# Optimization experiments

Measured on AMD Instinct MI355X. Metric: run time of the kernel, lower is better.

Reference implementation:

```python
import jax, jax.numpy as jnp
import numpy as np

N_NODES = 100000
N_EDGES = 1600000
IN_CH = 256
HID = 128   # latent_dim * 2
LAT = 64    # latent_dim


def _gcn_conv(x, W, b, src, dst, n_nodes):
    """PyG GCNConv: linear -> symmetric degree-norm scatter-add -> bias.
    src/dst already include self-loops."""
    h = x @ W.T                                             # [N, out]
    deg = jax.ops.segment_sum(jnp.ones_like(dst, dtype=h.dtype), dst,
                              num_segments=n_nodes)          # in-degree incl. self-loop
    dinv = jnp.where(deg > 0, jax.lax.rsqrt(deg), 0.0)
    norm = dinv[src] * dinv[dst]                             # [E]
    msg = h[src] * norm[:, None]                             # gather + scale, [E, out]
    out = jax.ops.segment_sum(msg, dst, num_segments=n_nodes)  # scatter-add
    return out + b


def setup_inputs() -> dict:
    key = jax.random.key(0)
    k1, k2, k3, k4, k5, k6 = jax.random.split(key, 6)
    x = jax.random.normal(k1, (N_NODES, IN_CH), dtype=jnp.float32)
    edge_index = jax.random.randint(k2, (2, N_EDGES), 0, N_NODES, dtype=jnp.int64)
    # Glorot-ish init for linear weights, zero bias (PyG default)
    W1 = jax.random.normal(k3, (HID, IN_CH), dtype=jnp.float32) / np.sqrt(IN_CH)
    b1 = jnp.zeros((HID,), dtype=jnp.float32)
    W2 = jax.random.normal(k4, (LAT, HID), dtype=jnp.float32) / np.sqrt(HID)
    b2 = jnp.zeros((LAT,), dtype=jnp.float32)
    return {"x": x, "edge_index": edge_index, "W1": W1, "b1": b1, "W2": W2, "b2": b2}


def reference(x, edge_index, W1, b1, W2, b2):
    n = x.shape[0]
    # add self-loops (PyG GCNConv default add_self_loops=True)
    loop = jnp.arange(n, dtype=edge_index.dtype)
    src = jnp.concatenate([edge_index[0], loop])
    dst = jnp.concatenate([edge_index[1], loop])
    h = jax.nn.relu(_gcn_conv(x, W1, b1, src, dst, n))
    return _gcn_conv(h, W2, b2, src, dst, n)
```

## Files before the change

### kernel.cpp

```cpp
#include <hip/hip_runtime.h>
#include <math.h>

constexpr int IN_CH = 256;
constexpr int HID   = 128;
constexpr int LAT   = 64;

constexpr int SBN    = 1024;
constexpr int SB_CAP = 18432;
constexpr int EPB    = 8192;
constexpr int HCAP   = 9472;

typedef unsigned short u16;
typedef unsigned int   u32;
typedef unsigned char  u8;
typedef __bf16  bf16x8 __attribute__((ext_vector_type(8)));
typedef float   f32x4  __attribute__((ext_vector_type(4)));

__device__ inline u16 f2bf(float f) {
    unsigned u = __float_as_uint(f);
    unsigned r = u + 0x7FFF + ((u >> 16) & 1);
    return (u16)(r >> 16);
}
__device__ inline float bf2f(u16 h) {
    return __uint_as_float((unsigned)h << 16);
}


__global__ void k_zero(int* p, int n) {
    int i = blockIdx.x * blockDim.x + threadIdx.x;
    if (i < n) p[i] = 0;
}

__launch_bounds__(512)
__global__ void k_bin_sb(const int* __restrict__ esrc, const int* __restrict__ edst,
                         int* __restrict__ sb_fill, u32* __restrict__ sbe,
                         int E, int NSB) {
    __shared__ u32 sorted[EPB];
    __shared__ u8  ssb[EPB];
    __shared__ int cnt[128], sc[128], excl[128], fil[128], off[128];

    const int t  = threadIdx.x;
    const int e0 = blockIdx.x * EPB;

    for (int j = t; j < 128; j += 512) { cnt[j] = 0; fil[j] = 0; }
    __syncthreads();

#pragma unroll
    for (int it = 0; it < EPB / 512; ++it) {
        int e = e0 + it * 512 + t;
        if (e < E) atomicAdd(&cnt[edst[e] >> 10], 1);
    }
    __syncthreads();

    if (t < 128) sc[t] = cnt[t];
    __syncthreads();
#pragma unroll
    for (int o = 1; o < 128; o <<= 1) {
        int u = 0;
        if (t < 128 && t >= o) u = sc[t - o];
        __syncthreads();
        if (t < 128) sc[t] += u;
        __syncthreads();
    }
    if (t < 128) excl[t] = sc[t] - cnt[t];
    if (t < NSB) off[t] = atomicAdd(&sb_fill[t], cnt[t]);
    __syncthreads();

#pragma unroll
    for (int it = 0; it < EPB / 512; ++it) {
        int e = e0 + it * 512 + t;
        if (e < E) {
            int d  = edst[e];
            int sb = d >> 10;
            int pos = excl[sb] + atomicAdd(&fil[sb], 1);
            sorted[pos] = (u32)esrc[e] | ((u32)(d & 1023) << 17);
            ssb[pos]    = (u8)sb;
        }
    }
    __syncthreads();

    int mtot = sc[127];
    for (int i = t; i < mtot; i += 512) {
        int sb = ssb[i];
        int o  = off[sb] + (i - excl[sb]);
        if (o < SB_CAP) sbe[(size_t)sb * SB_CAP + o] = sorted[i];
    }
}

__launch_bounds__(512)
__global__ void k_sbsort(const int* __restrict__ sb_fill, const u32* __restrict__ sbe,
                         int* __restrict__ csr, int* __restrict__ row_ptr,
                         int* __restrict__ row_end, float* __restrict__ dinv, int N) {
    __shared__ int cnt[SBN];
    __shared__ int exclh[512];
    __shared__ int fillb[512];
    __shared__ int lsrc[HCAP];
    __shared__ int wsum[8];
    __shared__ int sh_h1base, sh_mtot;

    const int t    = threadIdx.x;
    const int sb   = blockIdx.x >> 1;
    const int half = blockIdx.x & 1;
    const int m    = min(sb_fill[sb], SB_CAP);
    const size_t base = (size_t)sb * SB_CAP;
    const int node0 = sb * SBN;

    for (int j = t; j < SBN; j += 512) cnt[j] = 0;
    fillb[t & 511] = 0;
    __syncthreads();

    for (int i = t; i < m; i += 512)
        atomicAdd(&cnt[sbe[base + i] >> 17], 1);
    __syncthreads();

    int c0 = cnt[2 * t], c1 = cnt[2 * t + 1];
    int p  = c0 + c1;
    int lane = t & 63, wid = t >> 6;
    int v = p;
#pragma unroll
    for (int o = 1; o < 64; o <<= 1) {
        int u = __shfl_up(v, o, 64);
        if (lane >= o) v += u;
    }
    if (lane == 63) wsum[wid] = v;
    __syncthreads();
    int woff = 0;
#pragma unroll
    for (int w = 0; w < 8; ++w) if (w < wid) woff += wsum[w];
    int incl = woff + v;
    int eP   = incl - p;
    if (t == 511) sh_mtot = incl;
    if (t == 256) sh_h1base = eP;

#pragma unroll
    for (int q = 0; q < 2; ++q) {
        int j  = 2 * t + q;
        int ex = q ? (eP + c0) : eP;
        int cc = q ? c1 : c0;
        if ((j >> 9) == half) {
            exclh[j & 511] = ex;
            int node = node0 + j;
            if (node < N) {
                row_ptr[node] = (int)base + ex;
                row_end[node] = (int)base + ex + cc;
                dinv[node]    = rsqrtf((float)(cc + 1));
            }
        }
    }
    __syncthreads();

    const int hb = (half == 0) ? 0 : sh_h1base;
    int mh = (half == 0) ? sh_h1base : (sh_mtot - sh_h1base);

    for (int i = t; i < m; i += 512) {
        u32 p2  = sbe[base + i];
        int d10 = p2 >> 17;
        if ((d10 >> 9) == half) {
            int slot = atomicAdd(&fillb[d10 & 511], 1);
            int pos  = exclh[d10 & 511] - hb + slot;
            if (pos < HCAP) lsrc[pos] = (int)(p2 & 0x1FFFF);
        }
    }
    __syncthreads();

    if (mh > HCAP) mh = HCAP;
    for (int i = t; i < mh; i += 512) csr[base + hb + i] = lsrc[i];
}


__global__ void k_split_w(const float* __restrict__ W, u16* __restrict__ Wh,
                          u16* __restrict__ Wl, int n) {
    int i = blockIdx.x * blockDim.x + threadIdx.x;
    if (i < n) {
        float v = W[i];
        u16 h = f2bf(v);
        Wh[i] = h;
        Wl[i] = f2bf(v - bf2f(h));
    }
}


template<int K, int NOUT, bool A_BF16, typename AT>
__device__ inline void gemm_body(int bid,
                                 const AT* __restrict__ A,
                                 const u16* __restrict__ Wh,
                                 const u16* __restrict__ Wl,
                                 const float* __restrict__ dinv,
                                 u16* __restrict__ h_out,
                                 int M) {
    constexpr int BM = 64, BK = 32, LDT = 40, THREADS = 512;
    constexpr int WAVES_N  = (NOUT == 128) ? 4 : 2;
    constexpr int WAVES_M  = 8 / WAVES_N;
    constexpr int WM       = BM / WAVES_M;
    constexpr int WN       = 32;
    constexpr int MF       = WM / 16;
    constexpr int NF       = WN / 16;

    __shared__ u16 Ah[BM][LDT];
    __shared__ u16 Al[A_BF16 ? 1 : BM][A_BF16 ? 1 : LDT];
    __shared__ u16 Bh[NOUT][LDT], Bl[NOUT][LDT];

    const int t    = threadIdx.x;
    const int lane = t & 63;
    const int wid  = t >> 6;
    const int wm   = (wid / WAVES_N) * WM;
    const int wn   = (wid % WAVES_N) * WN;
    const int lr   = lane & 15;
    const int lk   = (lane >> 4) * 8;
    const int row0 = bid * BM;

    f32x4 acc[MF][NF];
#pragma unroll
    for (int i = 0; i < MF; ++i)
#pragma unroll
        for (int j = 0; j < NF; ++j) acc[i][j] = (f32x4)(0.f);

    for (int k0 = 0; k0 < K; k0 += BK) {
        {
            int r  = t >> 3;
            int c4 = (t & 7) * 4;
            int gr = row0 + r;
            if (A_BF16) {
                ushort4 hv = make_ushort4(0, 0, 0, 0);
                if (gr < M) hv = *(const ushort4*)&((const u16*)A)[(size_t)gr * K + k0 + c4];
                *(ushort4*)&Ah[r][c4] = hv;
            } else {
                float4 v = make_float4(0.f, 0.f, 0.f, 0.f);
                if (gr < M) v = *(const float4*)&((const float*)A)[(size_t)gr * K + k0 + c4];
                ushort4 hi, lo;
                hi.x = f2bf(v.x); lo.x = f2bf(v.x - bf2f(hi.x));
                hi.y = f2bf(v.y); lo.y = f2bf(v.y - bf2f(hi.y));
                hi.z = f2bf(v.z); lo.z = f2bf(v.z - bf2f(hi.z));
                hi.w = f2bf(v.w); lo.w = f2bf(v.w - bf2f(hi.w));
                *(ushort4*)&Ah[r][c4] = hi;
                *(ushort4*)&Al[r][c4] = lo;
            }
        }
#pragma unroll
        for (int it = 0; it < (NOUT * BK / 4) / THREADS; ++it) {
            int q  = it * THREADS + t;
            int r  = q >> 3;
            int c4 = (q & 7) * 4;
            *(ushort4*)&Bh[r][c4] = *(const ushort4*)&Wh[(size_t)r * K + k0 + c4];
            *(ushort4*)&Bl[r][c4] = *(const ushort4*)&Wl[(size_t)r * K + k0 + c4];
        }
        __syncthreads();

        bf16x8 ah[MF], al[MF], bh[NF], bl[NF];
#pragma unroll
        for (int mf = 0; mf < MF; ++mf) {
            ah[mf] = *(const bf16x8*)&Ah[wm + mf * 16 + lr][lk];
            if (!A_BF16) al[mf] = *(const bf16x8*)&Al[wm + mf * 16 + lr][lk];
        }
#pragma unroll
        for (int nf = 0; nf < NF; ++nf) {
            bh[nf] = *(const bf16x8*)&Bh[wn + nf * 16 + lr][lk];
            bl[nf] = *(const bf16x8*)&Bl[wn + nf * 16 + lr][lk];
        }
#pragma unroll
        for (int mf = 0; mf < MF; ++mf)
#pragma unroll
            for (int nf = 0; nf < NF; ++nf) {
                acc[mf][nf] = __builtin_amdgcn_mfma_f32_16x16x32_bf16(ah[mf], bh[nf], acc[mf][nf], 0, 0, 0);
                acc[mf][nf] = __builtin_amdgcn_mfma_f32_16x16x32_bf16(ah[mf], bl[nf], acc[mf][nf], 0, 0, 0);
                if (!A_BF16)
                    acc[mf][nf] = __builtin_amdgcn_mfma_f32_16x16x32_bf16(al[mf], bh[nf], acc[mf][nf], 0, 0, 0);
            }
        __syncthreads();
    }

#pragma unroll
    for (int mf = 0; mf < MF; ++mf) {
#pragma unroll
        for (int r = 0; r < 4; ++r) {
            int grow = row0 + wm + mf * 16 + (lane >> 4) * 4 + r;
            if (grow < M) {
                float dv = dinv[grow];
#pragma unroll
                for (int nf = 0; nf < NF; ++nf)
                    h_out[(size_t)grow * NOUT + wn + nf * 16 + lr] = f2bf(acc[mf][nf][r] * dv);
            }
        }
    }
}

__launch_bounds__(512, 4)
__global__ void k_gemm1(const float* __restrict__ A,
                        const u16* __restrict__ Wh, const u16* __restrict__ Wl,
                        const float* __restrict__ dinv, u16* __restrict__ h_out, int M) {
    gemm_body<IN_CH, HID, false>(blockIdx.x, A, Wh, Wl, dinv, h_out, M);
}

__launch_bounds__(512, 4)
__global__ void k_gemm2(const u16* __restrict__ A,
                        const u16* __restrict__ Wh, const u16* __restrict__ Wl,
                        const float* __restrict__ dinv, u16* __restrict__ h_out, int M) {
    gemm_body<HID, LAT, true>(blockIdx.x, A, Wh, Wl, dinv, h_out, M);
}


__device__ inline void acc8(float* a, uint4 v) {
    a[0] += __uint_as_float(v.x << 16);
    a[1] += __uint_as_float(v.x & 0xFFFF0000u);
    a[2] += __uint_as_float(v.y << 16);
    a[3] += __uint_as_float(v.y & 0xFFFF0000u);
    a[4] += __uint_as_float(v.z << 16);
    a[5] += __uint_as_float(v.z & 0xFFFF0000u);
    a[6] += __uint_as_float(v.w << 16);
    a[7] += __uint_as_float(v.w & 0xFFFF0000u);
}

template<int C, bool RELU, bool OUT_BF16>
__global__ void k_aggregate(const int* __restrict__ row_ptr,
                            const int* __restrict__ row_end,
                            const int* __restrict__ csr,
                            const u16* __restrict__ h,
                            const float* __restrict__ dinv,
                            const float* __restrict__ bias,
                            void* __restrict__ out_v, int n) {
    constexpr int QSHIFT = (C == 128) ? 4 : 3;
    long long tid = (long long)blockIdx.x * blockDim.x + threadIdx.x;
    int node = (int)(tid >> QSHIFT);
    if (node >= n) return;
    int c = ((int)tid & ((1 << QSHIFT) - 1)) * 8;

    int k   = row_ptr[node];
    int end = row_end[node];

    float a[8] = {0.f, 0.f, 0.f, 0.f, 0.f, 0.f, 0.f, 0.f};
    acc8(a, *(const uint4*)&h[(size_t)node * C + c]);

    for (; k + 8 <= end; k += 8) {
        int s0 = csr[k],     s1 = csr[k + 1], s2 = csr[k + 2], s3 = csr[k + 3];
        int s4 = csr[k + 4], s5 = csr[k + 5], s6 = csr[k + 6], s7 = csr[k + 7];
        uint4 v0 = *(const uint4*)&h[(size_t)s0 * C + c];
        uint4 v1 = *(const uint4*)&h[(size_t)s1 * C + c];
        uint4 v2 = *(const uint4*)&h[(size_t)s2 * C + c];
        uint4 v3 = *(const uint4*)&h[(size_t)s3 * C + c];
        uint4 v4 = *(const uint4*)&h[(size_t)s4 * C + c];
        uint4 v5 = *(const uint4*)&h[(size_t)s5 * C + c];
        uint4 v6 = *(const uint4*)&h[(size_t)s6 * C + c];
        uint4 v7 = *(const uint4*)&h[(size_t)s7 * C + c];
        acc8(a, v0); acc8(a, v1); acc8(a, v2); acc8(a, v3);
        acc8(a, v4); acc8(a, v5); acc8(a, v6); acc8(a, v7);
    }
    if (k + 4 <= end) {
        int s0 = csr[k], s1 = csr[k + 1], s2 = csr[k + 2], s3 = csr[k + 3];
        uint4 v0 = *(const uint4*)&h[(size_t)s0 * C + c];
        uint4 v1 = *(const uint4*)&h[(size_t)s1 * C + c];
        uint4 v2 = *(const uint4*)&h[(size_t)s2 * C + c];
        uint4 v3 = *(const uint4*)&h[(size_t)s3 * C + c];
        acc8(a, v0); acc8(a, v1); acc8(a, v2); acc8(a, v3);
        k += 4;
    }
    for (; k < end; ++k) {
        int s0 = csr[k];
        acc8(a, *(const uint4*)&h[(size_t)s0 * C + c]);
    }

    float dvn = dinv[node];
    float4 b0 = *(const float4*)&bias[c];
    float4 b1 = *(const float4*)&bias[c + 4];
    float o[8];
    o[0] = fmaf(a[0], dvn, b0.x);
    o[1] = fmaf(a[1], dvn, b0.y);
    o[2] = fmaf(a[2], dvn, b0.z);
    o[3] = fmaf(a[3], dvn, b0.w);
    o[4] = fmaf(a[4], dvn, b1.x);
    o[5] = fmaf(a[5], dvn, b1.y);
    o[6] = fmaf(a[6], dvn, b1.z);
    o[7] = fmaf(a[7], dvn, b1.w);
    if (RELU) {
#pragma unroll
        for (int j = 0; j < 8; ++j) o[j] = fmaxf(o[j], 0.f);
    }
    if (OUT_BF16) {
        u16 r[8];
#pragma unroll
        for (int j = 0; j < 8; ++j) r[j] = f2bf(o[j]);
        *(uint4*)&((u16*)out_v)[(size_t)node * C + c] = *(const uint4*)r;
    } else {
        float* out = (float*)out_v;
        *(f32x4*)&out[(size_t)node * C + c]     = *(const f32x4*)&o[0];
        *(f32x4*)&out[(size_t)node * C + c + 4] = *(const f32x4*)&o[4];
    }
}


extern "C" void kernel_launch(void* const* d_in, const int* in_sizes, int n_in,
                              void* d_out, int out_size, void* d_ws, size_t ws_size,
                              hipStream_t stream) {
    const float* x   = (const float*)d_in[0];
    const int*   ei  = (const int*)d_in[1];
    const float* W1  = (const float*)d_in[2];
    const float* b1  = (const float*)d_in[3];
    const float* W2  = (const float*)d_in[4];
    const float* b2  = (const float*)d_in[5];
    float*       out = (float*)d_out;

    const int N = in_sizes[0] / IN_CH;
    const int E = in_sizes[1] / 2;
    const int* esrc = ei;
    const int* edst = ei + E;

    const int NSB = (N + SBN - 1) / SBN;
    const int NBB = (E + EPB - 1) / EPB;
    const int GB  = (N + 63) / 64;

    char* ws = (char*)d_ws;
    int*   sb_fill = (int*)ws;    ws += (size_t)((NSB + 31) & ~31) * 4;
    u32*   sbe     = (u32*)ws;    ws += (size_t)NSB * SB_CAP * 4;
    int*   csr     = (int*)ws;    ws += (size_t)NSB * SB_CAP * 4;
    int*   row_ptr = (int*)ws;    ws += (size_t)N * 4;
    int*   row_end = (int*)ws;    ws += (size_t)N * 4;
    float* dinv    = (float*)ws;  ws += (size_t)N * 4;
    u16*   W1h     = (u16*)ws;    ws += (size_t)HID * IN_CH * 2;
    u16*   W1l     = (u16*)ws;    ws += (size_t)HID * IN_CH * 2;
    u16*   W2h     = (u16*)ws;    ws += (size_t)LAT * HID * 2;
    u16*   W2l     = (u16*)ws;    ws += (size_t)LAT * HID * 2;
    u16*   h1      = (u16*)ws;    ws += (size_t)N * HID * 2;
    u16*   h2      = (u16*)ws;    ws += (size_t)N * LAT * 2;
    u16*   out1    = (u16*)ws;    ws += (size_t)N * HID * 2;

    dim3 blk(256);

    k_zero   <<<1, 128, 0, stream>>>(sb_fill, NSB);
    k_split_w<<<(HID * IN_CH + 255) / 256, blk, 0, stream>>>(W1, W1h, W1l, HID * IN_CH);
    k_split_w<<<(LAT * HID + 255) / 256, blk, 0, stream>>>(W2, W2h, W2l, LAT * HID);

    k_bin_sb<<<NBB, dim3(512), 0, stream>>>(esrc, edst, sb_fill, sbe, E, NSB);
    k_sbsort<<<NSB * 2, dim3(512), 0, stream>>>(sb_fill, sbe, csr, row_ptr, row_end, dinv, N);

    k_gemm1<<<GB, dim3(512), 0, stream>>>(x, W1h, W1l, dinv, h1, N);
    {
        long long tot = (long long)N * 16;
        k_aggregate<HID, true, true><<<(unsigned)((tot + 255) / 256), blk, 0, stream>>>(
            row_ptr, row_end, csr, h1, dinv, b1, out1, N);
    }

    k_gemm2<<<GB, dim3(512), 0, stream>>>(out1, W2h, W2l, dinv, h2, N);
    {
        long long tot = (long long)N * 8;
        k_aggregate<LAT, false, false><<<(unsigned)((tot + 255) / 256), blk, 0, stream>>>(
            row_ptr, row_end, csr, h2, dinv, b2, out, N);
    }
}
```

Measured before the change: 197.6 us.

## Double-buffer GEMM shared-memory tiles with register prefetch of next K tile

The GEMM K loop now keeps two shared-memory buffers and loads the next K tile from global memory into registers before the current tile's MFMA work, writing it to the other buffer afterward. This hides global load latency behind matrix math and removes one barrier per iteration. In exchange it doubles LDS use and raises register pressure, which could lower occupancy under the 512-thread, 4-block launch bounds. The GEMM is likely only part of total time, since the scatter/gather stages probably dominate.

```diff
diff --git a/kernel.cpp b/kernel.cpp
--- a/kernel.cpp
+++ b/kernel.cpp
@@ -195,10 +195,11 @@
     constexpr int WN       = 32;
     constexpr int MF       = WM / 16;
     constexpr int NF       = WN / 16;
-
-    __shared__ u16 Ah[BM][LDT];
-    __shared__ u16 Al[A_BF16 ? 1 : BM][A_BF16 ? 1 : LDT];
-    __shared__ u16 Bh[NOUT][LDT], Bl[NOUT][LDT];
+    constexpr int BIT      = (NOUT * BK / 4) / THREADS;
+
+    __shared__ u16 AhS[2][BM][LDT];
+    __shared__ u16 AlS[A_BF16 ? 1 : 2][A_BF16 ? 1 : BM][A_BF16 ? 1 : LDT];
+    __shared__ u16 BhS[2][NOUT][LDT], BlS[2][NOUT][LDT];
 
     const int t    = threadIdx.x;
     const int lane = t & 63;
@@ -209,53 +210,79 @@
     const int lk   = (lane >> 4) * 8;
     const int row0 = bid * BM;
 
+    const int ar  = t >> 3;
+    const int ac4 = (t & 7) * 4;
+    const int gr  = row0 + ar;
+
     f32x4 acc[MF][NF];
 #pragma unroll
     for (int i = 0; i < MF; ++i)
 #pragma unroll
         for (int j = 0; j < NF; ++j) acc[i][j] = (f32x4)(0.f);
 
-    for (int k0 = 0; k0 < K; k0 += BK) {
-        {
-            int r  = t >> 3;
-            int c4 = (t & 7) * 4;
-            int gr = row0 + r;
-            if (A_BF16) {
-                ushort4 hv = make_ushort4(0, 0, 0, 0);
-                if (gr < M) hv = *(const ushort4*)&((const u16*)A)[(size_t)gr * K + k0 + c4];
-                *(ushort4*)&Ah[r][c4] = hv;
-            } else {
-                float4 v = make_float4(0.f, 0.f, 0.f, 0.f);
-                if (gr < M) v = *(const float4*)&((const float*)A)[(size_t)gr * K + k0 + c4];
-                ushort4 hi, lo;
-                hi.x = f2bf(v.x); lo.x = f2bf(v.x - bf2f(hi.x));
-                hi.y = f2bf(v.y); lo.y = f2bf(v.y - bf2f(hi.y));
-                hi.z = f2bf(v.z); lo.z = f2bf(v.z - bf2f(hi.z));
-                hi.w = f2bf(v.w); lo.w = f2bf(v.w - bf2f(hi.w));
-                *(ushort4*)&Ah[r][c4] = hi;
-                *(ushort4*)&Al[r][c4] = lo;
-            }
-        }
-#pragma unroll
-        for (int it = 0; it < (NOUT * BK / 4) / THREADS; ++it) {
+    float4  av;
+    ushort4 ahv;
+    ushort4 bhv[BIT], blv[BIT];
+
+    auto load_tile = [&](int k0) {
+        if constexpr (A_BF16) {
+            ahv = make_ushort4(0, 0, 0, 0);
+            if (gr < M) ahv = *(const ushort4*)&((const u16*)A)[(size_t)gr * K + k0 + ac4];
+        } else {
+            av = make_float4(0.f, 0.f, 0.f, 0.f);
+            if (gr < M) av = *(const float4*)&((const float*)A)[(size_t)gr * K + k0 + ac4];
+        }
+#pragma unroll
+        for (int it = 0; it < BIT; ++it) {
             int q  = it * THREADS + t;
             int r  = q >> 3;
             int c4 = (q & 7) * 4;
-            *(ushort4*)&Bh[r][c4] = *(const ushort4*)&Wh[(size_t)r * K + k0 + c4];
-            *(ushort4*)&Bl[r][c4] = *(const ushort4*)&Wl[(size_t)r * K + k0 + c4];
-        }
-        __syncthreads();
+            bhv[it] = *(const ushort4*)&Wh[(size_t)r * K + k0 + c4];
+            blv[it] = *(const ushort4*)&Wl[(size_t)r * K + k0 + c4];
+        }
+    };
+    auto write_tile = [&](int buf) {
+        if constexpr (A_BF16) {
+            *(ushort4*)&AhS[buf][ar][ac4] = ahv;
+        } else {
+            ushort4 hi, lo;
+            hi.x = f2bf(av.x); lo.x = f2bf(av.x - bf2f(hi.x));
+            hi.y = f2bf(av.y); lo.y = f2bf(av.y - bf2f(hi.y));
+            hi.z = f2bf(av.z); lo.z = f2bf(av.z - bf2f(hi.z));
+            hi.w = f2bf(av.w); lo.w = f2bf(av.w - bf2f(hi.w));
+            *(ushort4*)&AhS[buf][ar][ac4] = hi;
+            *(ushort4*)&AlS[buf][ar][ac4] = lo;
+        }
+#pragma unroll
+        for (int it = 0; it < BIT; ++it) {
+            int q  = it * THREADS + t;
+            int r  = q >> 3;
+            int c4 = (q & 7) * 4;
+            *(ushort4*)&BhS[buf][r][c4] = bhv[it];
+            *(ushort4*)&BlS[buf][r][c4] = blv[it];
+        }
+    };
+
+    load_tile(0);
+    write_tile(0);
+    __syncthreads();
+
+    int cur = 0;
+    for (int k0 = 0; k0 < K; k0 += BK) {
+        const bool have_next = (k0 + BK < K);
+        if (have_next) load_tile(k0 + BK);
 
         bf16x8 ah[MF], al[MF], bh[NF], bl[NF];
 #pragma unroll
         for (int mf = 0; mf < MF; ++mf) {
-            ah[mf] = *(const bf16x8*)&Ah[wm + mf * 16 + lr][lk];
-            if (!A_BF16) al[mf] = *(const bf16x8*)&Al[wm + mf * 16 + lr][lk];
+            ah[mf] = *(const bf16x8*)&AhS[cur][wm + mf * 16 + lr][lk];
+            if constexpr (!A_BF16)
+                al[mf] = *(const bf16x8*)&AlS[cur][wm + mf * 16 + lr][lk];
         }
 #pragma unroll
         for (int nf = 0; nf < NF; ++nf) {
-            bh[nf] = *(const bf16x8*)&Bh[wn + nf * 16 + lr][lk];
-            bl[nf] = *(const bf16x8*)&Bl[wn + nf * 16 + lr][lk];
+            bh[nf] = *(const bf16x8*)&BhS[cur][wn + nf * 16 + lr][lk];
+            bl[nf] = *(const bf16x8*)&BlS[cur][wn + nf * 16 + lr][lk];
         }
 #pragma unroll
         for (int mf = 0; mf < MF; ++mf)
@@ -263,10 +290,13 @@
             for (int nf = 0; nf < NF; ++nf) {
                 acc[mf][nf] = __builtin_amdgcn_mfma_f32_16x16x32_bf16(ah[mf], bh[nf], acc[mf][nf], 0, 0, 0);
                 acc[mf][nf] = __builtin_amdgcn_mfma_f32_16x16x32_bf16(ah[mf], bl[nf], acc[mf][nf], 0, 0, 0);
-                if (!A_BF16)
+                if constexpr (!A_BF16)
                     acc[mf][nf] = __builtin_amdgcn_mfma_f32_16x16x32_bf16(al[mf], bh[nf], acc[mf][nf], 0, 0, 0);
             }
+
+        if (have_next) write_tile(cur ^ 1);
         __syncthreads();
+        cur ^= 1;
     }
 
 #pragma unroll
```

Measured after the change: 199.4 us. No clear change (+0.9%).

## Keep GCN weights resident in LDS with persistent per-wave 16-row GEMM strips

Applied to the files above, without the earlier changes.

The two tiled GEMM kernels are replaced by one persistent kernel. Each 1024-thread block loads the whole split (high/low bf16) weight matrix into LDS once. Each wave then loops over 16-row strips, reading A straight from global memory into registers with a one-step software prefetch. This removes the repeated per-tile staging of weights and A through LDS and the per-k barriers. In exchange, gemm1 needs a large LDS footprint (about 135 KB), which limits occupancy to one block per CU, and A reads become per-lane row fragments rather than coalesced tile loads.

```diff
diff --git a/kernel.cpp b/kernel.cpp
--- a/kernel.cpp
+++ b/kernel.cpp
@@ -181,121 +181,103 @@
 
 
 template<int K, int NOUT, bool A_BF16, typename AT>
-__device__ inline void gemm_body(int bid,
-                                 const AT* __restrict__ A,
-                                 const u16* __restrict__ Wh,
-                                 const u16* __restrict__ Wl,
-                                 const float* __restrict__ dinv,
-                                 u16* __restrict__ h_out,
-                                 int M) {
-    constexpr int BM = 64, BK = 32, LDT = 40, THREADS = 512;
-    constexpr int WAVES_N  = (NOUT == 128) ? 4 : 2;
-    constexpr int WAVES_M  = 8 / WAVES_N;
-    constexpr int WM       = BM / WAVES_M;
-    constexpr int WN       = 32;
-    constexpr int MF       = WM / 16;
-    constexpr int NF       = WN / 16;
-
-    __shared__ u16 Ah[BM][LDT];
-    __shared__ u16 Al[A_BF16 ? 1 : BM][A_BF16 ? 1 : LDT];
-    __shared__ u16 Bh[NOUT][LDT], Bl[NOUT][LDT];
+__launch_bounds__(1024, 4)
+__global__ void k_gemm_wres(const AT* __restrict__ A,
+                            const u16* __restrict__ Wh,
+                            const u16* __restrict__ Wl,
+                            const float* __restrict__ dinv,
+                            u16* __restrict__ h_out,
+                            int M) {
+    constexpr int LDK = K + 8;
+    constexpr int NF  = NOUT / 16;
+
+    __shared__ u16 Bh[NOUT][LDK], Bl[NOUT][LDK];
 
     const int t    = threadIdx.x;
     const int lane = t & 63;
     const int wid  = t >> 6;
-    const int wm   = (wid / WAVES_N) * WM;
-    const int wn   = (wid % WAVES_N) * WN;
     const int lr   = lane & 15;
     const int lk   = (lane >> 4) * 8;
-    const int row0 = bid * BM;
-
-    f32x4 acc[MF][NF];
-#pragma unroll
-    for (int i = 0; i < MF; ++i)
-#pragma unroll
-        for (int j = 0; j < NF; ++j) acc[i][j] = (f32x4)(0.f);
-
-    for (int k0 = 0; k0 < K; k0 += BK) {
-        {
-            int r  = t >> 3;
-            int c4 = (t & 7) * 4;
-            int gr = row0 + r;
-            if (A_BF16) {
-                ushort4 hv = make_ushort4(0, 0, 0, 0);
-                if (gr < M) hv = *(const ushort4*)&((const u16*)A)[(size_t)gr * K + k0 + c4];
-                *(ushort4*)&Ah[r][c4] = hv;
+
+    constexpr int CH = NOUT * (K / 8);
+    for (int q = t; q < CH; q += 1024) {
+        int r  = q / (K / 8);
+        int c8 = (q % (K / 8)) * 8;
+        *(uint4*)&Bh[r][c8] = *(const uint4*)&Wh[(size_t)r * K + c8];
+        *(uint4*)&Bl[r][c8] = *(const uint4*)&Wl[(size_t)r * K + c8];
+    }
+    __syncthreads();
+
+    const int NS     = (M + 15) >> 4;
+    const int stride = (int)gridDim.x << 4;
+
+    for (int s = ((int)blockIdx.x << 4) + wid; s < NS; s += stride) {
+        const int row0 = s << 4;
+        const int arow = min(row0 + lr, M - 1);
+        const AT* ap = A + (size_t)arow * K + lk;
+
+        f32x4 acc[NF];
+#pragma unroll
+        for (int i = 0; i < NF; ++i) acc[i] = (f32x4)(0.f);
+
+        float4 a0, a1;
+        uint4  ab;
+        if constexpr (A_BF16) {
+            ab = *(const uint4*)ap;
+        } else {
+            a0 = *(const float4*)ap;
+            a1 = *(const float4*)(ap + 4);
+        }
+
+#pragma unroll
+        for (int k0 = 0; k0 < K; k0 += 32) {
+            float4 n0 = a0, n1 = a1;
+            uint4  nb = ab;
+            if (k0 + 32 < K) {
+                if constexpr (A_BF16) {
+                    nb = *(const uint4*)(ap + k0 + 32);
+                } else {
+                    n0 = *(const float4*)(ap + k0 + 32);
+                    n1 = *(const float4*)(ap + k0 + 36);
+                }
+            }
+
+            bf16x8 ah, al;
+            if constexpr (A_BF16) {
+                ah = *(bf16x8*)&ab;
             } else {
-                float4 v = make_float4(0.f, 0.f, 0.f, 0.f);
-                if (gr < M) v = *(const float4*)&((const float*)A)[(size_t)gr * K + k0 + c4];
-                ushort4 hi, lo;
-                hi.x = f2bf(v.x); lo.x = f2bf(v.x - bf2f(hi.x));
-                hi.y = f2bf(v.y); lo.y = f2bf(v.y - bf2f(hi.y));
-                hi.z = f2bf(v.z); lo.z = f2bf(v.z - bf2f(hi.z));
-                hi.w = f2bf(v.w); lo.w = f2bf(v.w - bf2f(hi.w));
-                *(ushort4*)&Ah[r][c4] = hi;
-                *(ushort4*)&Al[r][c4] = lo;
+                float f[8] = {a0.x, a0.y, a0.z, a0.w, a1.x, a1.y, a1.z, a1.w};
+#pragma unroll
+                for (int j = 0; j < 8; ++j) {
+                    __bf16 h = (__bf16)f[j];
+                    ah[j] = h;
+                    al[j] = (__bf16)(f[j] - (float)h);
+                }
             }
-        }
-#pragma unroll
-        for (int it = 0; it < (NOUT * BK / 4) / THREADS; ++it) {
-            int q  = it * THREADS + t;
-            int r  = q >> 3;
-            int c4 = (q & 7) * 4;
-            *(ushort4*)&Bh[r][c4] = *(const ushort4*)&Wh[(size_t)r * K + k0 + c4];
-            *(ushort4*)&Bl[r][c4] = *(const ushort4*)&Wl[(size_t)r * K + k0 + c4];
-        }
-        __syncthreads();
-
-        bf16x8 ah[MF], al[MF], bh[NF], bl[NF];
-#pragma unroll
-        for (int mf = 0; mf < MF; ++mf) {
-            ah[mf] = *(const bf16x8*)&Ah[wm + mf * 16 + lr][lk];
-            if (!A_BF16) al[mf] = *(const bf16x8*)&Al[wm + mf * 16 + lr][lk];
-        }
-#pragma unroll
-        for (int nf = 0; nf < NF; ++nf) {
-            bh[nf] = *(const bf16x8*)&Bh[wn + nf * 16 + lr][lk];
-            bl[nf] = *(const bf16x8*)&Bl[wn + nf * 16 + lr][lk];
-        }
-#pragma unroll
-        for (int mf = 0; mf < MF; ++mf)
+
 #pragma unroll
             for (int nf = 0; nf < NF; ++nf) {
-                acc[mf][nf] = __builtin_amdgcn_mfma_f32_16x16x32_bf16(ah[mf], bh[nf], acc[mf][nf], 0, 0, 0);
-                acc[mf][nf] = __builtin_amdgcn_mfma_f32_16x16x32_bf16(ah[mf], bl[nf], acc[mf][nf], 0, 0, 0);
-                if (!A_BF16)
-                    acc[mf][nf] = __builtin_amdgcn_mfma_f32_16x16x32_bf16(al[mf], bh[nf], acc[mf][nf], 0, 0, 0);
+                bf16x8 bh = *(const bf16x8*)&Bh[nf * 16 + lr][k0 + lk];
+                bf16x8 bl = *(const bf16x8*)&Bl[nf * 16 + lr][k0 + lk];
+                acc[nf] = __builtin_amdgcn_mfma_f32_16x16x32_bf16(ah, bh, acc[nf], 0, 0, 0);
+                acc[nf] = __builtin_amdgcn_mfma_f32_16x16x32_bf16(ah, bl, acc[nf], 0, 0, 0);
+                if constexpr (!A_BF16)
+                    acc[nf] = __builtin_amdgcn_mfma_f32_16x16x32_bf16(al, bh, acc[nf], 0, 0, 0);
             }
-        __syncthreads();
-    }
-
-#pragma unroll
-    for (int mf = 0; mf < MF; ++mf) {
+            a0 = n0; a1 = n1; ab = nb;
+        }
+
 #pragma unroll
         for (int r = 0; r < 4; ++r) {
-            int grow = row0 + wm + mf * 16 + (lane >> 4) * 4 + r;
+            int grow = row0 + ((lane >> 4) << 2) + r;
             if (grow < M) {
                 float dv = dinv[grow];
 #pragma unroll
                 for (int nf = 0; nf < NF; ++nf)
-                    h_out[(size_t)grow * NOUT + wn + nf * 16 + lr] = f2bf(acc[mf][nf][r] * dv);
+                    h_out[(size_t)grow * NOUT + nf * 16 + lr] = f2bf(acc[nf][r] * dv);
             }
         }
     }
-}
-
-__launch_bounds__(512, 4)
-__global__ void k_gemm1(const float* __restrict__ A,
-                        const u16* __restrict__ Wh, const u16* __restrict__ Wl,
-                        const float* __restrict__ dinv, u16* __restrict__ h_out, int M) {
-    gemm_body<IN_CH, HID, false>(blockIdx.x, A, Wh, Wl, dinv, h_out, M);
-}
-
-__launch_bounds__(512, 4)
-__global__ void k_gemm2(const u16* __restrict__ A,
-                        const u16* __restrict__ Wh, const u16* __restrict__ Wl,
-                        const float* __restrict__ dinv, u16* __restrict__ h_out, int M) {
-    gemm_body<HID, LAT, true>(blockIdx.x, A, Wh, Wl, dinv, h_out, M);
 }
 
 
@@ -405,7 +387,6 @@
 
     const int NSB = (N + SBN - 1) / SBN;
     const int NBB = (E + EPB - 1) / EPB;
-    const int GB  = (N + 63) / 64;
 
     char* ws = (char*)d_ws;
     int*   sb_fill = (int*)ws;    ws += (size_t)((NSB + 31) & ~31) * 4;
@@ -431,14 +412,16 @@
     k_bin_sb<<<NBB, dim3(512), 0, stream>>>(esrc, edst, sb_fill, sbe, E, NSB);
     k_sbsort<<<NSB * 2, dim3(512), 0, stream>>>(sb_fill, sbe, csr, row_ptr, row_end, dinv, N);
 
-    k_gemm1<<<GB, dim3(512), 0, stream>>>(x, W1h, W1l, dinv, h1, N);
+    k_gemm_wres<IN_CH, HID, false, float><<<256, dim3(1024), 0, stream>>>(
+        x, W1h, W1l, dinv, h1, N);
     {
         long long tot = (long long)N * 16;
         k_aggregate<HID, true, true><<<(unsigned)((tot + 255) / 256), blk, 0, stream>>>(
             row_ptr, row_end, csr, h1, dinv, b1, out1, N);
     }
 
-    k_gemm2<<<GB, dim3(512), 0, stream>>>(out1, W2h, W2l, dinv, h2, N);
+    k_gemm_wres<HID, LAT, true, u16><<<512, dim3(1024), 0, stream>>>(
+        out1, W2h, W2l, dinv, h2, N);
     {
         long long tot = (long long)N * 8;
         k_aggregate<LAT, false, false><<<(unsigned)((tot + 255) / 256), blk, 0, stream>>>(
```

Result: slower. 514.4 us (+160.3%).
